# Performance work log

Hardware: AMD Instinct MI355X
Metric: run time of the kernel (lower is better)

The kernel has to match this reference:

```python
import jax, jax.numpy as jnp
import numpy as np

D = 1024
LN_EPS = 1e-5


def setup_inputs() -> dict:
    key = jax.random.key(0)
    k1, k2 = jax.random.split(key)
    L, B = 2048, 8
    x = jax.random.normal(k1, (L, B, D), dtype=jnp.float32)
    c = jnp.zeros((B, D), dtype=jnp.float32)
    W = jax.random.normal(k2, (3 * D, D), dtype=jnp.float32) * (1.0 / np.sqrt(D))
    # bias: forget-gate slice [D:2D] initialized to 1.5, rest zero (matches _init_bias)
    b = jnp.zeros((3 * D,), dtype=jnp.float32).at[D:2 * D].set(1.5)
    ln_g = jnp.ones((D,), dtype=jnp.float32)
    ln_b = jnp.zeros((D,), dtype=jnp.float32)
    return {"x": x, "c": c, "W": W, "b": b, "ln_g": ln_g, "ln_b": ln_b}


def _layernorm(x, g, b):
    mu = jnp.mean(x, axis=-1, keepdims=True)
    var = jnp.mean(jnp.square(x - mu), axis=-1, keepdims=True)
    return (x - mu) * jax.lax.rsqrt(var + LN_EPS) * g + b


def _sru_forward(x, c, W, b, ln_g, ln_b):
    residual = x
    x_norm = _layernorm(x, ln_g, ln_b)          # [L, B, D]
    ufr = jnp.einsum('lbd,ed->lbe', x_norm, W) + b  # [L, B, 3D]
    u, f, r = jnp.split(ufr, 3, axis=-1)
    f_gate = jax.nn.sigmoid(f)
    r_gate = jax.nn.sigmoid(r)
    u_tanh = jnp.tanh(u)

    def step(c_prev, inputs):
        f_t, u_t = inputs
        c_t = f_t * c_prev + (1.0 - f_t) * u_t
        return c_t, c_t

    last_c, c_stack = jax.lax.scan(step, c, (f_gate, u_tanh))  # [L, B, D]
    hs = r_gate * jnp.tanh(c_stack) + (1.0 - r_gate) * x_norm
    return residual + hs, last_c


def reference(x, c, W, b, ln_g, ln_b):
    return _sru_forward(x, c, W, b, ln_g, ln_b)
```

## Files before the change

### kernel.cpp

```cpp
#include <hip/hip_runtime.h>

#define L_DIM 2048
#define B_DIM 8
#define DD    1024
#define M_DIM 16384
#define N_DIM 3072
#define K_DIM 1024
#define CH    8192
#define CH8   1024
#define NSEG  128
#define LSEG  16
#define LN_EPS 1e-5f

typedef __attribute__((ext_vector_type(8))) short bf16x8;
typedef __attribute__((ext_vector_type(8))) unsigned short u16x8;
typedef __attribute__((ext_vector_type(4))) float f32x4;

__device__ __forceinline__ unsigned short f2bf(float f){
  unsigned u = __float_as_uint(f);
  u += 0x7fffu + ((u >> 16) & 1u);
  return (unsigned short)(u >> 16);
}
__device__ __forceinline__ float bf2f(unsigned short h){
  return __uint_as_float(((unsigned)h) << 16);
}
__device__ __forceinline__ float fsigmoid(float z){ return 1.0f/(1.0f + __expf(-z)); }
__device__ __forceinline__ float ftanh(float z){ return 1.0f - 2.0f/(1.0f + __expf(2.0f*z)); }

__global__ __launch_bounds__(256) void ln_kernel(const float* __restrict__ x,
                                                 const float* __restrict__ g,
                                                 const float* __restrict__ bta,
                                                 unsigned short* __restrict__ xn)
{
  int tid  = threadIdx.x;
  int wave = tid >> 6, lane = tid & 63;
  int row  = blockIdx.x * 4 + wave;
  const float4* xr = (const float4*)(x + (size_t)row * DD);
  float4 v[4];
  #pragma unroll
  for (int k = 0; k < 4; k++) v[k] = xr[lane + k * 64];
  float s = 0.f, sq = 0.f;
  #pragma unroll
  for (int k = 0; k < 4; k++) {
    s  += v[k].x + v[k].y + v[k].z + v[k].w;
    sq += v[k].x*v[k].x + v[k].y*v[k].y + v[k].z*v[k].z + v[k].w*v[k].w;
  }
  #pragma unroll
  for (int off = 32; off > 0; off >>= 1) {
    s  += __shfl_down(s,  off, 64);
    sq += __shfl_down(sq, off, 64);
  }
  s  = __shfl(s,  0, 64);
  sq = __shfl(sq, 0, 64);
  float mean = s * (1.0f / DD);
  float var  = sq * (1.0f / DD) - mean * mean;
  float rstd = rsqrtf(var + LN_EPS);
  ushort4* xo = (ushort4*)(xn + (size_t)row * DD);
  #pragma unroll
  for (int k = 0; k < 4; k++) {
    float4 gg = ((const float4*)g)[lane + k * 64];
    float4 bb = ((const float4*)bta)[lane + k * 64];
    ushort4 o;
    o.x = f2bf((v[k].x - mean) * rstd * gg.x + bb.x);
    o.y = f2bf((v[k].y - mean) * rstd * gg.y + bb.y);
    o.z = f2bf((v[k].z - mean) * rstd * gg.z + bb.z);
    o.w = f2bf((v[k].w - mean) * rstd * gg.w + bb.w);
    xo[lane + k * 64] = o;
  }
}

__global__ __launch_bounds__(256) void wconv_kernel(const float* __restrict__ W,
                                                    unsigned short* __restrict__ wb)
{
  int gid = blockIdx.x * 256 + threadIdx.x;
  float4 v = ((const float4*)W)[gid];
  ushort4 o;
  o.x = f2bf(v.x); o.y = f2bf(v.y); o.z = f2bf(v.z); o.w = f2bf(v.w);
  ((ushort4*)wb)[gid] = o;
}

#define BM 256
#define BN 128
#define BK 64
#define NT 16
#define LDP 136

#define GLDS16(gp, lp) __builtin_amdgcn_global_load_lds( \
    (const __attribute__((address_space(1))) void*)(gp), \
    (__attribute__((address_space(3))) void*)(lp), 16, 0, 0)

#define SBAR()   __builtin_amdgcn_s_barrier()
#define SCHED0() __builtin_amdgcn_sched_barrier(0)
#define WAIT_LGKM(N) do { asm volatile("s_waitcnt lgkmcnt(" #N ")" ::: "memory"); SCHED0(); } while(0)
#define WAIT_VM(N)   do { asm volatile("s_waitcnt vmcnt(" #N ")" ::: "memory"); SCHED0(); } while(0)

#define DSR(dst, addr, IMM) \
  asm volatile("ds_read_b128 %0, %1 offset:" #IMM : "=v"(dst) : "v"(addr))

#define MFMA(a, b, c) __builtin_amdgcn_mfma_f32_16x16x32_bf16((a), (b), (c), 0, 0, 0)

__global__ __launch_bounds__(512, 4) void gemm_gates(const unsigned short* __restrict__ A,
                                                     const unsigned short* __restrict__ Bw,
                                                     const float* __restrict__ bias,
                                                     unsigned short* __restrict__ u_t,
                                                     unsigned short* __restrict__ f_g,
                                                     unsigned short* __restrict__ r_g)
{
  __shared__ unsigned short smem[40960];
  const int tid  = threadIdx.x;
  const int wave = tid >> 6, lane = tid & 63;

  const int bm0 = blockIdx.x * BM;
  const int bn0 = blockIdx.y * BN;

  f32x4 zero = {0.f, 0.f, 0.f, 0.f};
  f32x4 acc[8][2];
  #pragma unroll
  for (int i = 0; i < 8; i++)
    #pragma unroll
    for (int j = 0; j < 2; j++) acc[i][j] = zero;

  const int q8  = lane >> 3;
  const int rr8 = lane & 7;
  const int sch = rr8 ^ q8;
  const unsigned short* a_lane = A  + (size_t)(bm0 + wave * 32 + q8) * K_DIM + sch * 8;
  const unsigned short* b_lane = Bw + (size_t)(bn0 + wave * 16 + q8) * K_DIM + sch * 8;

  const int wm = (wave >> 2) * 128, wn = (wave & 3) * 32;
  const int fm = lane & 15, quad = lane >> 4;
  const int f7 = fm & 7;

#define STAGE_A(BUF, T) do { \
  GLDS16(a_lane + (size_t)(T) * BK,                      &smem[(BUF)*16384 + (wave * 32 +  0) * BK]); \
  GLDS16(a_lane + (size_t)(T) * BK + (size_t) 8 * K_DIM, &smem[(BUF)*16384 + (wave * 32 +  8) * BK]); \
  GLDS16(a_lane + (size_t)(T) * BK + (size_t)16 * K_DIM, &smem[(BUF)*16384 + (wave * 32 + 16) * BK]); \
  GLDS16(a_lane + (size_t)(T) * BK + (size_t)24 * K_DIM, &smem[(BUF)*16384 + (wave * 32 + 24) * BK]); \
} while(0)

#define STAGE_B(T) do { \
  GLDS16(b_lane + (size_t)(T) * BK,                      &smem[32768 + (wave * 16 + 0) * BK]); \
  GLDS16(b_lane + (size_t)(T) * BK + (size_t) 8 * K_DIM, &smem[32768 + (wave * 16 + 8) * BK]); \
} while(0)

#define COMPUTE_KK(AADDR, BADDR) do { \
  bf16x8 b0f, b1f, a0f, a1f, a2f, a3f; \
  DSR(b0f, (BADDR), 0); DSR(b1f, (BADDR), 2048); \
  DSR(a0f, (AADDR), 0);    DSR(a1f, (AADDR), 2048); \
  DSR(a2f, (AADDR), 4096); DSR(a3f, (AADDR), 6144); \
  WAIT_LGKM(2);  \
  acc[0][0] = MFMA(a0f, b0f, acc[0][0]); acc[0][1] = MFMA(a0f, b1f, acc[0][1]); \
  acc[1][0] = MFMA(a1f, b0f, acc[1][0]); acc[1][1] = MFMA(a1f, b1f, acc[1][1]); \
  WAIT_LGKM(0);  \
  acc[2][0] = MFMA(a2f, b0f, acc[2][0]); acc[2][1] = MFMA(a2f, b1f, acc[2][1]); \
  acc[3][0] = MFMA(a3f, b0f, acc[3][0]); acc[3][1] = MFMA(a3f, b1f, acc[3][1]); \
  DSR(a0f, (AADDR), 8192);  DSR(a1f, (AADDR), 10240); \
  DSR(a2f, (AADDR), 12288); DSR(a3f, (AADDR), 14336); \
  WAIT_LGKM(2);  \
  acc[4][0] = MFMA(a0f, b0f, acc[4][0]); acc[4][1] = MFMA(a0f, b1f, acc[4][1]); \
  acc[5][0] = MFMA(a1f, b0f, acc[5][0]); acc[5][1] = MFMA(a1f, b1f, acc[5][1]); \
  WAIT_LGKM(0); \
  acc[6][0] = MFMA(a2f, b0f, acc[6][0]); acc[6][1] = MFMA(a2f, b1f, acc[6][1]); \
  acc[7][0] = MFMA(a3f, b0f, acc[7][0]); acc[7][1] = MFMA(a3f, b1f, acc[7][1]); \
} while(0)

  const unsigned slot0 = (unsigned)((quad ^ f7) << 4);
  const unsigned aBase = (unsigned)((wm + fm) * 128) + slot0;
  const unsigned bBase = 65536u + (unsigned)((wn + fm) * 128) + slot0;

  STAGE_B(0);
  STAGE_A(0, 0);
  STAGE_A(1, 1);
  WAIT_VM(4);
  SBAR();

  #pragma unroll
  for (int t = 0; t < NT; ++t) {
    const int cb = t & 1;
    const unsigned cbB = (unsigned)(cb * 32768);
    COMPUTE_KK(cbB + aBase,         bBase);
    COMPUTE_KK((cbB + aBase) ^ 64u, bBase ^ 64u);
    SCHED0();
    SBAR();
    if (t + 1 < NT) STAGE_B(t + 1);
    if (t + 2 < NT) STAGE_A(cb, t + 2);
    SCHED0();
    if      (t <  NT - 2) WAIT_VM(4);
    else if (t == NT - 2) WAIT_VM(0);
    SBAR();
  }
  __syncthreads();

  const int slice = bn0 >> 10;
  const int nd0   = bn0 & 1023;
  unsigned short* dst = (slice == 0) ? u_t : ((slice == 1) ? f_g : r_g);

  #pragma unroll
  for (int h = 0; h < 2; ++h) {
    if ((wave >> 2) == h) {
      #pragma unroll
      for (int ni = 0; ni < 2; ni++) {
        int lcol = wn + ni * 16 + fm;
        float bia = bias[bn0 + lcol];
        #pragma unroll
        for (int mi = 0; mi < 8; mi++) {
          #pragma unroll
          for (int reg = 0; reg < 4; reg++) {
            int lrow = mi * 16 + quad * 4 + reg;
            float v = acc[mi][ni][reg] + bia;
            float act = (slice == 0) ? ftanh(v) : fsigmoid(v);
            smem[lrow * LDP + lcol] = f2bf(act);
          }
        }
      }
    }
    __syncthreads();
    #pragma unroll
    for (int it = 0; it < 4; ++it) {
      int row = it * 32 + (tid >> 4);
      int cc  = (tid & 15) * 8;
      u16x8 v = *(const u16x8*)&smem[row * LDP + cc];
      *(u16x8*)(dst + (size_t)(bm0 + h * 128 + row) * DD + nd0 + cc) = v;
    }
    __syncthreads();
  }
}

__global__ __launch_bounds__(256) void scan_pass1(const unsigned short* __restrict__ f_g,
                                                  const unsigned short* __restrict__ u_t,
                                                  unsigned short* __restrict__ P,
                                                  unsigned short* __restrict__ E)
{
  int vc8 = blockIdx.x * 256 + threadIdx.x;
  int seg = blockIdx.y;
  const u16x8* f8 = (const u16x8*)f_g;
  const u16x8* u8 = (const u16x8*)u_t;
  size_t g = (size_t)(seg * LSEG) * CH8 + vc8;
  float p[8], e[8];
  #pragma unroll
  for (int k = 0; k < 8; k++) { p[k] = 1.f; e[k] = 0.f; }
  #pragma unroll 4
  for (int i = 0; i < LSEG; i++) {
    u16x8 ff = f8[g];
    u16x8 uu = u8[g];
    #pragma unroll
    for (int k = 0; k < 8; k++) {
      float fv = bf2f(ff[k]);
      e[k] = fv * e[k] + (1.f - fv) * bf2f(uu[k]);
      p[k] *= fv;
    }
    g += CH8;
  }
  u16x8 pv, ev;
  #pragma unroll
  for (int k = 0; k < 8; k++) { pv[k] = f2bf(p[k]); ev[k] = f2bf(e[k]); }
  ((u16x8*)P)[(size_t)seg * CH8 + vc8] = pv;
  ((u16x8*)E)[(size_t)seg * CH8 + vc8] = ev;
}

__global__ __launch_bounds__(128) void scan_pass2(const unsigned short* __restrict__ P,
                                                  const unsigned short* __restrict__ E,
                                                  const float* __restrict__ c0,
                                                  float* __restrict__ Cini,
                                                  float* __restrict__ lastc)
{
  int ch = blockIdx.x * 128 + threadIdx.x;
  float c = c0[ch];
  #pragma unroll 8
  for (int s = 0; s < NSEG; s++) {
    Cini[(size_t)s * CH + ch] = c;
    c = bf2f(P[(size_t)s * CH + ch]) * c + bf2f(E[(size_t)s * CH + ch]);
  }
  lastc[ch] = c;
}

__global__ __launch_bounds__(256) void scan_pass3(const unsigned short* __restrict__ f_g,
                                                  const unsigned short* __restrict__ u_t,
                                                  const unsigned short* __restrict__ r_g,
                                                  const float* __restrict__ x,
                                                  const unsigned short* __restrict__ xn,
                                                  const float* __restrict__ Cini,
                                                  float* __restrict__ out)
{
  int vc8 = blockIdx.x * 256 + threadIdx.x;
  int seg = blockIdx.y;
  const u16x8* f8 = (const u16x8*)f_g;
  const u16x8* u8 = (const u16x8*)u_t;
  const u16x8* r8 = (const u16x8*)r_g;
  const u16x8* n8 = (const u16x8*)xn;
  const float4* x4 = (const float4*)x;
  float4* o4 = (float4*)out;
  float c[8];
  {
    const float4* C4 = (const float4*)Cini;
    size_t ci = (size_t)seg * (CH / 4) + (size_t)vc8 * 2;
    float4 ca = C4[ci], cb = C4[ci + 1];
    c[0]=ca.x; c[1]=ca.y; c[2]=ca.z; c[3]=ca.w;
    c[4]=cb.x; c[5]=cb.y; c[6]=cb.z; c[7]=cb.w;
  }
  size_t g = (size_t)(seg * LSEG) * CH8 + vc8;
  #pragma unroll 2
  for (int i = 0; i < LSEG; i++) {
    u16x8 ff = f8[g];
    u16x8 uu = u8[g];
    u16x8 rr = r8[g];
    u16x8 nn = n8[g];
    size_t xi = g * 2;
    float4 xa = x4[xi], xb = x4[xi + 1];
    float ov[8];
    #pragma unroll
    for (int k = 0; k < 8; k++) {
      float fv = bf2f(ff[k]);
      c[k] = fv * c[k] + (1.f - fv) * bf2f(uu[k]);
      float rv = bf2f(rr[k]);
      ov[k] = rv * ftanh(c[k]) + (1.f - rv) * bf2f(nn[k]);
    }
    o4[xi]     = (float4){xa.x + ov[0], xa.y + ov[1], xa.z + ov[2], xa.w + ov[3]};
    o4[xi + 1] = (float4){xb.x + ov[4], xb.y + ov[5], xb.z + ov[6], xb.w + ov[7]};
    g += CH8;
  }
}

extern "C" void kernel_launch(void* const* d_in, const int* in_sizes, int n_in,
                              void* d_out, int out_size, void* d_ws, size_t ws_size,
                              hipStream_t stream) {
  const float* x    = (const float*)d_in[0];
  const float* c0   = (const float*)d_in[1];
  const float* W    = (const float*)d_in[2];
  const float* bias = (const float*)d_in[3];
  const float* ln_g = (const float*)d_in[4];
  const float* ln_b = (const float*)d_in[5];
  float* out = (float*)d_out;

  char* ws = (char*)d_ws;
  unsigned short* xn  = (unsigned short*)(ws);
  unsigned short* wb  = (unsigned short*)(ws + 33554432ULL);
  unsigned short* u_t = (unsigned short*)(ws + 39845888ULL);
  unsigned short* f_g = (unsigned short*)(ws + 73400320ULL);
  unsigned short* r_g = (unsigned short*)(ws + 106954752ULL);
  unsigned short* Pseg = (unsigned short*)(ws + 33554432ULL);
  unsigned short* Eseg = (unsigned short*)(ws + 35651584ULL);
  float* Cini = (float*)(ws + 140509184ULL);

  ln_kernel   <<<M_DIM / 4, 256, 0, stream>>>(x, ln_g, ln_b, xn);
  wconv_kernel<<<N_DIM, 256, 0, stream>>>(W, wb);
  gemm_gates  <<<dim3(M_DIM / BM, N_DIM / BN), 512, 0, stream>>>(xn, wb, bias, u_t, f_g, r_g);
  scan_pass1  <<<dim3(CH8 / 256, NSEG), 256, 0, stream>>>(f_g, u_t, Pseg, Eseg);
  scan_pass2  <<<CH / 128, 128, 0, stream>>>(Pseg, Eseg, c0, Cini, out + (size_t)M_DIM * DD);
  scan_pass3  <<<dim3(CH8 / 256, NSEG), 256, 0, stream>>>(f_g, u_t, r_g, x, xn, Cini, out);
}
```

Before: 205.8 us.

## Fuse LN and weight conversion launches; split B tile staging into K halves

Merges the layernorm and weight bf16 conversion kernels into one launch with disjoint block ranges, saving a kernel launch. In the GEMM main loop, B tile staging is split into two K-halves with a new swizzled layout. Each half is reloaded after its compute phase, with a barrier between the two COMPUTE_KK calls. This aims to overlap B loads with compute, but adds an extra barrier and a full vmcnt(0) wait per iteration, which may stall the A-tile prefetch.

```diff
diff --git a/kernel.cpp b/kernel.cpp
--- a/kernel.cpp
+++ b/kernel.cpp
@@ -27,12 +27,22 @@
 __device__ __forceinline__ float fsigmoid(float z){ return 1.0f/(1.0f + __expf(-z)); }
 __device__ __forceinline__ float ftanh(float z){ return 1.0f - 2.0f/(1.0f + __expf(2.0f*z)); }
 
-__global__ __launch_bounds__(256) void ln_kernel(const float* __restrict__ x,
-                                                 const float* __restrict__ g,
-                                                 const float* __restrict__ bta,
-                                                 unsigned short* __restrict__ xn)
+__global__ __launch_bounds__(256) void ln_wconv_kernel(const float* __restrict__ x,
+                                                       const float* __restrict__ g,
+                                                       const float* __restrict__ bta,
+                                                       unsigned short* __restrict__ xn,
+                                                       const float* __restrict__ W,
+                                                       unsigned short* __restrict__ wb)
 {
   int tid  = threadIdx.x;
+  if (blockIdx.x >= M_DIM / 4) {
+    int gid = (blockIdx.x - M_DIM / 4) * 256 + tid;
+    float4 v = ((const float4*)W)[gid];
+    ushort4 o;
+    o.x = f2bf(v.x); o.y = f2bf(v.y); o.z = f2bf(v.z); o.w = f2bf(v.w);
+    ((ushort4*)wb)[gid] = o;
+    return;
+  }
   int wave = tid >> 6, lane = tid & 63;
   int row  = blockIdx.x * 4 + wave;
   const float4* xr = (const float4*)(x + (size_t)row * DD);
@@ -69,16 +79,6 @@
   }
 }
 
-__global__ __launch_bounds__(256) void wconv_kernel(const float* __restrict__ W,
-                                                    unsigned short* __restrict__ wb)
-{
-  int gid = blockIdx.x * 256 + threadIdx.x;
-  float4 v = ((const float4*)W)[gid];
-  ushort4 o;
-  o.x = f2bf(v.x); o.y = f2bf(v.y); o.z = f2bf(v.z); o.w = f2bf(v.w);
-  ((ushort4*)wb)[gid] = o;
-}
-
 #define BM 256
 #define BN 128
 #define BK 64
@@ -123,8 +123,9 @@
   const int q8  = lane >> 3;
   const int rr8 = lane & 7;
   const int sch = rr8 ^ q8;
-  const unsigned short* a_lane = A  + (size_t)(bm0 + wave * 32 + q8) * K_DIM + sch * 8;
-  const unsigned short* b_lane = Bw + (size_t)(bn0 + wave * 16 + q8) * K_DIM + sch * 8;
+  const unsigned short* a_lane = A + (size_t)(bm0 + wave * 32 + q8) * K_DIM + sch * 8;
+  const unsigned short* b_src = Bw + (size_t)(bn0 + wave * 16 + (lane >> 2)) * K_DIM
+                                   + (size_t)(((lane & 3) ^ ((lane >> 2) & 3)) * 8);
 
   const int wm = (wave >> 2) * 128, wn = (wave & 3) * 32;
   const int fm = lane & 15, quad = lane >> 4;
@@ -137,25 +138,23 @@
   GLDS16(a_lane + (size_t)(T) * BK + (size_t)24 * K_DIM, &smem[(BUF)*16384 + (wave * 32 + 24) * BK]); \
 } while(0)
 
-#define STAGE_B(T) do { \
-  GLDS16(b_lane + (size_t)(T) * BK,                      &smem[32768 + (wave * 16 + 0) * BK]); \
-  GLDS16(b_lane + (size_t)(T) * BK + (size_t) 8 * K_DIM, &smem[32768 + (wave * 16 + 8) * BK]); \
-} while(0)
+#define STAGE_HA(T) GLDS16(b_src + (size_t)(T) * BK,      &smem[32768 + wave * 512])
+#define STAGE_HB(T) GLDS16(b_src + (size_t)(T) * BK + 32, &smem[36864 + wave * 512])
 
 #define COMPUTE_KK(AADDR, BADDR) do { \
   bf16x8 b0f, b1f, a0f, a1f, a2f, a3f; \
-  DSR(b0f, (BADDR), 0); DSR(b1f, (BADDR), 2048); \
+  DSR(b0f, (BADDR), 0); DSR(b1f, (BADDR), 1024); \
   DSR(a0f, (AADDR), 0);    DSR(a1f, (AADDR), 2048); \
   DSR(a2f, (AADDR), 4096); DSR(a3f, (AADDR), 6144); \
-  WAIT_LGKM(2);  \
+  WAIT_LGKM(2); \
   acc[0][0] = MFMA(a0f, b0f, acc[0][0]); acc[0][1] = MFMA(a0f, b1f, acc[0][1]); \
   acc[1][0] = MFMA(a1f, b0f, acc[1][0]); acc[1][1] = MFMA(a1f, b1f, acc[1][1]); \
-  WAIT_LGKM(0);  \
+  WAIT_LGKM(0); \
   acc[2][0] = MFMA(a2f, b0f, acc[2][0]); acc[2][1] = MFMA(a2f, b1f, acc[2][1]); \
   acc[3][0] = MFMA(a3f, b0f, acc[3][0]); acc[3][1] = MFMA(a3f, b1f, acc[3][1]); \
   DSR(a0f, (AADDR), 8192);  DSR(a1f, (AADDR), 10240); \
   DSR(a2f, (AADDR), 12288); DSR(a3f, (AADDR), 14336); \
-  WAIT_LGKM(2);  \
+  WAIT_LGKM(2); \
   acc[4][0] = MFMA(a0f, b0f, acc[4][0]); acc[4][1] = MFMA(a0f, b1f, acc[4][1]); \
   acc[5][0] = MFMA(a1f, b0f, acc[5][0]); acc[5][1] = MFMA(a1f, b1f, acc[5][1]); \
   WAIT_LGKM(0); \
@@ -165,9 +164,11 @@
 
   const unsigned slot0 = (unsigned)((quad ^ f7) << 4);
   const unsigned aBase = (unsigned)((wm + fm) * 128) + slot0;
-  const unsigned bBase = 65536u + (unsigned)((wn + fm) * 128) + slot0;
-
-  STAGE_B(0);
+  const unsigned bH = 65536u + (unsigned)((wn + fm) * 64)
+                             + (unsigned)((quad ^ (fm & 3)) << 4);
+
+  STAGE_HA(0);
+  STAGE_HB(0);
   STAGE_A(0, 0);
   STAGE_A(1, 1);
   WAIT_VM(4);
@@ -177,16 +178,18 @@
   for (int t = 0; t < NT; ++t) {
     const int cb = t & 1;
     const unsigned cbB = (unsigned)(cb * 32768);
-    COMPUTE_KK(cbB + aBase,         bBase);
-    COMPUTE_KK((cbB + aBase) ^ 64u, bBase ^ 64u);
+    COMPUTE_KK(cbB + aBase, bH);
+    if (t < NT - 1) { WAIT_VM(4); }
+    else           { WAIT_VM(0); }
+    SBAR();
+    if (t + 1 < NT) STAGE_HA(t + 1);
     SCHED0();
+    COMPUTE_KK((cbB + aBase) ^ 64u, bH + 8192u);
+    WAIT_VM(0);
     SBAR();
-    if (t + 1 < NT) STAGE_B(t + 1);
+    if (t + 1 < NT) STAGE_HB(t + 1);
     if (t + 2 < NT) STAGE_A(cb, t + 2);
     SCHED0();
-    if      (t <  NT - 2) WAIT_VM(4);
-    else if (t == NT - 2) WAIT_VM(0);
-    SBAR();
   }
   __syncthreads();
 
@@ -341,8 +344,7 @@
   unsigned short* Eseg = (unsigned short*)(ws + 35651584ULL);
   float* Cini = (float*)(ws + 140509184ULL);
 
-  ln_kernel   <<<M_DIM / 4, 256, 0, stream>>>(x, ln_g, ln_b, xn);
-  wconv_kernel<<<N_DIM, 256, 0, stream>>>(W, wb);
+  ln_wconv_kernel<<<M_DIM / 4 + N_DIM, 256, 0, stream>>>(x, ln_g, ln_b, xn, W, wb);
   gemm_gates  <<<dim3(M_DIM / BM, N_DIM / BN), 512, 0, stream>>>(xn, wb, bias, u_t, f_g, r_g);
   scan_pass1  <<<dim3(CH8 / 256, NSEG), 256, 0, stream>>>(f_g, u_t, Pseg, Eseg);
   scan_pass2  <<<CH / 128, 128, 0, stream>>>(Pseg, Eseg, c0, Cini, out + (size_t)M_DIM * DD);
```

Measured after the change: 202.5 us. Within noise of the previous version (-1.6%).

## Switch gate GEMM to 32x32x16 MFMA and fuse LN with weight conversion

Applied to the files above, without the earlier changes.

The gate GEMM now uses 32x32x16 bf16 MFMA tiles instead of 16x16x32, with four larger accumulators per wave. Each 64-wide K tile is split into four 16-wide sub-steps, and the LDS swizzle and epilogue row mapping are rewritten to match. The goal is fewer LDS reads per FLOP and fewer MFMA issues. Separately, the layernorm and weight-to-bf16 conversion kernels are merged into one launch, saving a kernel launch, at the cost of an extra branch in every block.

```diff
diff --git a/kernel.cpp b/kernel.cpp
--- a/kernel.cpp
+++ b/kernel.cpp
@@ -15,6 +15,7 @@
 typedef __attribute__((ext_vector_type(8))) short bf16x8;
 typedef __attribute__((ext_vector_type(8))) unsigned short u16x8;
 typedef __attribute__((ext_vector_type(4))) float f32x4;
+typedef __attribute__((ext_vector_type(16))) float f32x16;
 
 __device__ __forceinline__ unsigned short f2bf(float f){
   unsigned u = __float_as_uint(f);
@@ -27,12 +28,22 @@
 __device__ __forceinline__ float fsigmoid(float z){ return 1.0f/(1.0f + __expf(-z)); }
 __device__ __forceinline__ float ftanh(float z){ return 1.0f - 2.0f/(1.0f + __expf(2.0f*z)); }
 
-__global__ __launch_bounds__(256) void ln_kernel(const float* __restrict__ x,
-                                                 const float* __restrict__ g,
-                                                 const float* __restrict__ bta,
-                                                 unsigned short* __restrict__ xn)
+__global__ __launch_bounds__(256) void ln_wconv_kernel(const float* __restrict__ x,
+                                                       const float* __restrict__ g,
+                                                       const float* __restrict__ bta,
+                                                       unsigned short* __restrict__ xn,
+                                                       const float* __restrict__ W,
+                                                       unsigned short* __restrict__ wb)
 {
   int tid  = threadIdx.x;
+  if (blockIdx.x >= M_DIM / 4) {
+    int gid = (blockIdx.x - M_DIM / 4) * 256 + tid;
+    float4 v = ((const float4*)W)[gid];
+    ushort4 o;
+    o.x = f2bf(v.x); o.y = f2bf(v.y); o.z = f2bf(v.z); o.w = f2bf(v.w);
+    ((ushort4*)wb)[gid] = o;
+    return;
+  }
   int wave = tid >> 6, lane = tid & 63;
   int row  = blockIdx.x * 4 + wave;
   const float4* xr = (const float4*)(x + (size_t)row * DD);
@@ -69,16 +80,6 @@
   }
 }
 
-__global__ __launch_bounds__(256) void wconv_kernel(const float* __restrict__ W,
-                                                    unsigned short* __restrict__ wb)
-{
-  int gid = blockIdx.x * 256 + threadIdx.x;
-  float4 v = ((const float4*)W)[gid];
-  ushort4 o;
-  o.x = f2bf(v.x); o.y = f2bf(v.y); o.z = f2bf(v.z); o.w = f2bf(v.w);
-  ((ushort4*)wb)[gid] = o;
-}
-
 #define BM 256
 #define BN 128
 #define BK 64
@@ -97,7 +98,7 @@
 #define DSR(dst, addr, IMM) \
   asm volatile("ds_read_b128 %0, %1 offset:" #IMM : "=v"(dst) : "v"(addr))
 
-#define MFMA(a, b, c) __builtin_amdgcn_mfma_f32_16x16x32_bf16((a), (b), (c), 0, 0, 0)
+#define MFMA32(a, b, c) __builtin_amdgcn_mfma_f32_32x32x16_bf16((a), (b), (c), 0, 0, 0)
 
 __global__ __launch_bounds__(512, 4) void gemm_gates(const unsigned short* __restrict__ A,
                                                      const unsigned short* __restrict__ Bw,
@@ -113,22 +114,18 @@
   const int bm0 = blockIdx.x * BM;
   const int bn0 = blockIdx.y * BN;
 
-  f32x4 zero = {0.f, 0.f, 0.f, 0.f};
-  f32x4 acc[8][2];
-  #pragma unroll
-  for (int i = 0; i < 8; i++)
-    #pragma unroll
-    for (int j = 0; j < 2; j++) acc[i][j] = zero;
+  f32x16 zero16 = {0.f,0.f,0.f,0.f,0.f,0.f,0.f,0.f,0.f,0.f,0.f,0.f,0.f,0.f,0.f,0.f};
+  f32x16 acc[4];
+  #pragma unroll
+  for (int i = 0; i < 4; i++) acc[i] = zero16;
 
   const int q8  = lane >> 3;
-  const int rr8 = lane & 7;
-  const int sch = rr8 ^ q8;
+  const int sch = (lane & 7) ^ q8;
   const unsigned short* a_lane = A  + (size_t)(bm0 + wave * 32 + q8) * K_DIM + sch * 8;
   const unsigned short* b_lane = Bw + (size_t)(bn0 + wave * 16 + q8) * K_DIM + sch * 8;
 
   const int wm = (wave >> 2) * 128, wn = (wave & 3) * 32;
-  const int fm = lane & 15, quad = lane >> 4;
-  const int f7 = fm & 7;
+  const int l31 = lane & 31, h5 = lane >> 5, l7 = lane & 7;
 
 #define STAGE_A(BUF, T) do { \
   GLDS16(a_lane + (size_t)(T) * BK,                      &smem[(BUF)*16384 + (wave * 32 +  0) * BK]); \
@@ -142,30 +139,22 @@
   GLDS16(b_lane + (size_t)(T) * BK + (size_t) 8 * K_DIM, &smem[32768 + (wave * 16 + 8) * BK]); \
 } while(0)
 
-#define COMPUTE_KK(AADDR, BADDR) do { \
-  bf16x8 b0f, b1f, a0f, a1f, a2f, a3f; \
-  DSR(b0f, (BADDR), 0); DSR(b1f, (BADDR), 2048); \
-  DSR(a0f, (AADDR), 0);    DSR(a1f, (AADDR), 2048); \
-  DSR(a2f, (AADDR), 4096); DSR(a3f, (AADDR), 6144); \
+#define COMPUTE_KSUB(AADDR, BADDR) do { \
+  bf16x8 bf_, a0f, a1f, a2f, a3f; \
+  DSR(bf_, (BADDR), 0); \
+  DSR(a0f, (AADDR), 0);    DSR(a1f, (AADDR), 4096); \
+  DSR(a2f, (AADDR), 8192); DSR(a3f, (AADDR), 12288); \
   WAIT_LGKM(2);  \
-  acc[0][0] = MFMA(a0f, b0f, acc[0][0]); acc[0][1] = MFMA(a0f, b1f, acc[0][1]); \
-  acc[1][0] = MFMA(a1f, b0f, acc[1][0]); acc[1][1] = MFMA(a1f, b1f, acc[1][1]); \
-  WAIT_LGKM(0);  \
-  acc[2][0] = MFMA(a2f, b0f, acc[2][0]); acc[2][1] = MFMA(a2f, b1f, acc[2][1]); \
-  acc[3][0] = MFMA(a3f, b0f, acc[3][0]); acc[3][1] = MFMA(a3f, b1f, acc[3][1]); \
-  DSR(a0f, (AADDR), 8192);  DSR(a1f, (AADDR), 10240); \
-  DSR(a2f, (AADDR), 12288); DSR(a3f, (AADDR), 14336); \
-  WAIT_LGKM(2);  \
-  acc[4][0] = MFMA(a0f, b0f, acc[4][0]); acc[4][1] = MFMA(a0f, b1f, acc[4][1]); \
-  acc[5][0] = MFMA(a1f, b0f, acc[5][0]); acc[5][1] = MFMA(a1f, b1f, acc[5][1]); \
+  acc[0] = MFMA32(a0f, bf_, acc[0]); \
+  acc[1] = MFMA32(a1f, bf_, acc[1]); \
   WAIT_LGKM(0); \
-  acc[6][0] = MFMA(a2f, b0f, acc[6][0]); acc[6][1] = MFMA(a2f, b1f, acc[6][1]); \
-  acc[7][0] = MFMA(a3f, b0f, acc[7][0]); acc[7][1] = MFMA(a3f, b1f, acc[7][1]); \
+  acc[2] = MFMA32(a2f, bf_, acc[2]); \
+  acc[3] = MFMA32(a3f, bf_, acc[3]); \
 } while(0)
 
-  const unsigned slot0 = (unsigned)((quad ^ f7) << 4);
-  const unsigned aBase = (unsigned)((wm + fm) * 128) + slot0;
-  const unsigned bBase = 65536u + (unsigned)((wn + fm) * 128) + slot0;
+  const unsigned sw0  = (unsigned)((h5 ^ l7) << 4);
+  const unsigned aBase = (unsigned)((wm + l31) * 128) + sw0;
+  const unsigned bBase = 65536u + (unsigned)((wn + l31) * 128) + sw0;
 
   STAGE_B(0);
   STAGE_A(0, 0);
@@ -176,9 +165,11 @@
   #pragma unroll
   for (int t = 0; t < NT; ++t) {
     const int cb = t & 1;
-    const unsigned cbB = (unsigned)(cb * 32768);
-    COMPUTE_KK(cbB + aBase,         bBase);
-    COMPUTE_KK((cbB + aBase) ^ 64u, bBase ^ 64u);
+    const unsigned aB = aBase + (unsigned)(cb * 32768);
+    COMPUTE_KSUB(aB,        bBase);
+    COMPUTE_KSUB(aB ^ 32u,  bBase ^ 32u);
+    COMPUTE_KSUB(aB ^ 64u,  bBase ^ 64u);
+    COMPUTE_KSUB(aB ^ 96u,  bBase ^ 96u);
     SCHED0();
     SBAR();
     if (t + 1 < NT) STAGE_B(t + 1);
@@ -197,19 +188,16 @@
   #pragma unroll
   for (int h = 0; h < 2; ++h) {
     if ((wave >> 2) == h) {
+      int lcol = wn + l31;
+      float bia = bias[bn0 + lcol];
       #pragma unroll
-      for (int ni = 0; ni < 2; ni++) {
-        int lcol = wn + ni * 16 + fm;
-        float bia = bias[bn0 + lcol];
+      for (int mi = 0; mi < 4; mi++) {
         #pragma unroll
-        for (int mi = 0; mi < 8; mi++) {
-          #pragma unroll
-          for (int reg = 0; reg < 4; reg++) {
-            int lrow = mi * 16 + quad * 4 + reg;
-            float v = acc[mi][ni][reg] + bia;
-            float act = (slice == 0) ? ftanh(v) : fsigmoid(v);
-            smem[lrow * LDP + lcol] = f2bf(act);
-          }
+        for (int reg = 0; reg < 16; reg++) {
+          int lrow = mi * 32 + (reg & 3) + 8 * (reg >> 2) + 4 * h5;
+          float v = acc[mi][reg] + bia;
+          float act = (slice == 0) ? ftanh(v) : fsigmoid(v);
+          smem[lrow * LDP + lcol] = f2bf(act);
         }
       }
     }
@@ -341,8 +329,7 @@
   unsigned short* Eseg = (unsigned short*)(ws + 35651584ULL);
   float* Cini = (float*)(ws + 140509184ULL);
 
-  ln_kernel   <<<M_DIM / 4, 256, 0, stream>>>(x, ln_g, ln_b, xn);
-  wconv_kernel<<<N_DIM, 256, 0, stream>>>(W, wb);
+  ln_wconv_kernel<<<M_DIM / 4 + N_DIM, 256, 0, stream>>>(x, ln_g, ln_b, xn, W, wb);
   gemm_gates  <<<dim3(M_DIM / BM, N_DIM / BN), 512, 0, stream>>>(xn, wb, bias, u_t, f_g, r_g);
   scan_pass1  <<<dim3(CH8 / 256, NSEG), 256, 0, stream>>>(f_g, u_t, Pseg, Eseg);
   scan_pass2  <<<CH / 128, 128, 0, stream>>>(Pseg, Eseg, c0, Cini, out + (size_t)M_DIM * DD);
```

New measurement: 215.9 us. +4.9%, slower.
